# Performance work log

Hardware: AMD Instinct MI355X
Metric: run time of the kernel (lower is better)

## Reference

```python
import jax, jax.numpy as jnp
import numpy as np

N, E, F_IN, G = 50000, 800000, 128, 256
LAYERS = [(128, 4, 64), (256, 4, 64), (256, 1, 64)]  # (fan_in, heads, per-head dim)


def setup_inputs() -> dict:
    key = jax.random.key(0)
    ks = iter(jax.random.split(key, 64))
    nrm = lambda shp, s=1.0: jax.random.normal(next(ks), shp, jnp.float32) * s
    d = {}
    d["x"] = nrm((N, F_IN))
    d["edge_index"] = jax.random.randint(next(ks), (2, E), 0, N, dtype=jnp.int32)
    d["batch"] = jnp.sort(jax.random.randint(next(ks), (N,), 0, G, dtype=jnp.int32))
    for i, (fin, h, c) in enumerate(LAYERS):
        d[f"w{i}"] = nrm((fin, h * c), 1.0 / np.sqrt(fin))
        d[f"asrc{i}"] = nrm((h, c), 0.1)
        d[f"adst{i}"] = nrm((h, c), 0.1)
        d[f"b{i}"] = nrm((h * c,), 0.1)
        d[f"g{i}"] = 1.0 + nrm((h * c,), 0.1)
        d[f"be{i}"] = nrm((h * c,), 0.1)
        d[f"m{i}"] = nrm((h * c,), 0.1)
        d[f"v{i}"] = jnp.abs(nrm((h * c,), 0.1)) + 1.0
    d["fc1w"] = nrm((192, 64), 1.0 / np.sqrt(192)); d["fc1b"] = nrm((64,), 0.1)
    d["fc2w"] = nrm((64, 32), 1.0 / np.sqrt(64));   d["fc2b"] = nrm((32,), 0.1)
    d["fc3w"] = nrm((32, 1), 1.0 / np.sqrt(32));    d["fc3b"] = nrm((1,), 0.1)
    return d


def _gat_layer(x, w, a_s, a_d, b, src, dst, n, heads):
    c = w.shape[1] // heads
    h = (x @ w).reshape(n, heads, c)                      # [N,H,C]
    al_s = jnp.sum(h * a_s[None], axis=-1)                # [N,H]
    al_d = jnp.sum(h * a_d[None], axis=-1)                # [N,H]
    e = jax.nn.leaky_relu(al_s[src] + al_d[dst], 0.2)     # [E',H]
    emax = jax.ops.segment_max(e, dst, num_segments=n)
    emax = jnp.where(jnp.isfinite(emax), emax, 0.0)
    ee = jnp.exp(e - emax[dst])
    den = jax.ops.segment_sum(ee, dst, num_segments=n)
    alpha = ee / (den[dst] + 1e-16)                       # edge softmax per dst node
    out = jax.ops.segment_sum(h[src] * alpha[..., None], dst, num_segments=n)
    return out.reshape(n, heads * c) + b


def _bn(x, g, be, m, v):
    return (x - m) * jax.lax.rsqrt(v + 1e-5) * g + be


def reference(x, edge_index, batch,
              w0, asrc0, adst0, b0, g0, be0, m0, v0,
              w1, asrc1, adst1, b1, g1, be1, m1, v1,
              w2, asrc2, adst2, b2, g2, be2, m2, v2,
              fc1w, fc1b, fc2w, fc2b, fc3w, fc3b):
    n = x.shape[0]
    loop = jnp.arange(n, dtype=edge_index.dtype)          # add_self_loops (PyG default)
    src = jnp.concatenate([edge_index[0], loop])
    dst = jnp.concatenate([edge_index[1], loop])
    layers = [(w0, asrc0, adst0, b0, g0, be0, m0, v0, 4),
              (w1, asrc1, adst1, b1, g1, be1, m1, v1, 4),
              (w2, asrc2, adst2, b2, g2, be2, m2, v2, 1)]
    for (w, a_s, a_d, b, g, be, m, v, heads) in layers:
        x = _gat_layer(x, w, a_s, a_d, b, src, dst, n, heads)
        x = jax.nn.elu(_bn(x, g, be, m, v))
    # multi-pool readout over graphs
    xsum = jax.ops.segment_sum(x, batch, num_segments=G)
    cnt = jax.ops.segment_sum(jnp.ones((n, 1), x.dtype), batch, num_segments=G)
    xmean = xsum / jnp.maximum(cnt, 1.0)
    xmax = jax.ops.segment_max(x, batch, num_segments=G)
    xmax = jnp.where(jnp.isfinite(xmax), xmax, 0.0)
    h = jnp.concatenate([xmean, xmax, xsum], axis=1)      # [G, 192]
    h = jax.nn.relu(h @ fc1w + fc1b)
    h = jax.nn.relu(h @ fc2w + fc2b)
    return h @ fc3w + fc3b                                # [G, 1]
```

## Files before the change

kernel.cpp:

```cpp
#include <hip/hip_runtime.h>
#include <hip/hip_fp16.h>

typedef unsigned short ushort_t;
typedef unsigned int uint_t;
typedef __attribute__((ext_vector_type(8))) _Float16 half8;
typedef __attribute__((ext_vector_type(4))) float f32x4;

#define NN 50000
#define NE 800000
#define NGR 256

typedef __attribute__((address_space(3))) unsigned int as3_u32;
typedef const __attribute__((address_space(1))) unsigned int as1_u32c;
__device__ __forceinline__ void gld16(const ushort_t* g, void* lds_base) {
    __builtin_amdgcn_global_load_lds((as1_u32c*)g, (as3_u32*)lds_base, 16, 0, 0);
}

__global__ void k_scan1(const int* __restrict__ deg, int* __restrict__ rowp,
                        int* __restrict__ bsum, int M) {
    __shared__ int sm[256];
    int t = threadIdx.x, i = blockIdx.x * 256 + t;
    int v = (i < M) ? deg[i] + 1 : 0;
    sm[t] = v; __syncthreads();
    for (int off = 1; off < 256; off <<= 1) {
        int x = (t >= off) ? sm[t - off] : 0;
        __syncthreads();
        sm[t] += x;
        __syncthreads();
    }
    if (i < M) rowp[i] = sm[t] - v;
    if (t == 255) bsum[blockIdx.x] = sm[255];
}

__global__ void k_scan2(int* bsum, int NB) {
    __shared__ int sm[256];
    int t = threadIdx.x;
    int v = (t < NB) ? bsum[t] : 0;
    sm[t] = v; __syncthreads();
    for (int off = 1; off < 256; off <<= 1) {
        int x = (t >= off) ? sm[t - off] : 0;
        __syncthreads();
        sm[t] += x;
        __syncthreads();
    }
    if (t < NB) bsum[t] = sm[t] - v;
}

__global__ void k_scan3(int* rowp, const int* __restrict__ bsum, int* __restrict__ cur,
                        int M, int total) {
    int i = blockIdx.x * 256 + threadIdx.x;
    if (i < M) { rowp[i] += bsum[blockIdx.x]; cur[i] = 0; }
    if (i == 0) rowp[M] = total;
}

__global__ void k_prep(const float* __restrict__ x0, __half* __restrict__ xf,
                       const float* __restrict__ W0, const float* __restrict__ W1,
                       const float* __restrict__ W2, __half* __restrict__ th,
                       const int* __restrict__ edst, int* __restrict__ deg) {
    int i = blockIdx.x * 256 + threadIdx.x;
    if (i < 1600000) {
        float4 v = ((const float4*)x0)[i];
        __half2 a = __floats2half2_rn(v.x, v.y);
        __half2 b = __floats2half2_rn(v.z, v.w);
        *(__half2*)(xf + i * 4) = a;
        *(__half2*)(xf + i * 4 + 2) = b;
    } else if (i < 1600000 + 114688) {
        int w = i - 1600000;
        const float* W; int K, NC, idx, base;
        if (w < 32768)      { W = W0; K = 128; NC = 256; idx = w;         base = 0; }
        else if (w < 98304) { W = W1; K = 256; NC = 256; idx = w - 32768; base = 32768; }
        else                { W = W2; K = 256; NC = 64;  idx = w - 98304; base = 98304; }
        int k = idx / NC, n = idx % NC;
        th[base + n * K + k] = __float2half(W[idx]);
    } else if (i < 1600000 + 114688 + NE) {
        atomicAdd(&deg[edst[i - 1714688]], 1);
    }
}

template<int KD, int BN>
__device__ __forceinline__ void gemm_body(int bx, int by,
    const __half* __restrict__ Ax, const __half* __restrict__ Bth,
    __half* __restrict__ Hout, const float* __restrict__ a_s,
    const float* __restrict__ a_d, float* __restrict__ als,
    float* __restrict__ ald, int H, int M, int NC) {
    constexpr int BM = 128, BK = 32;
    __shared__ ushort_t sA[BM * BK];
    __shared__ ushort_t sB[BN * BK];
    const int tid = threadIdx.x;
    const int m0 = bx * BM;
    const int n0 = by * BN;
    const int wv = tid >> 6, ln = tid & 63;
    const int lrow = ln & 15, lq = ln >> 4;
    constexpr int RT = (BN == 128) ? 4 : 2;
    int wm, wn;
    if constexpr (BN == 128) { wm = (wv >> 1) * 64; wn = (wv & 1) * 64; }
    else                     { wm = wv * 32;        wn = 0; }
    const int roff = ln >> 2;
    const int coff = (ln & 3) * 8;

    f32x4 acc[RT][4] = {};

    for (int k0 = 0; k0 < KD; k0 += BK) {
        #pragma unroll
        for (int ch = 0; ch < 2; ++ch) {
            int rb = wv * 32 + ch * 16;
            size_t ga = (size_t)(m0 + rb + roff) * KD + k0 + coff;
            gld16((const ushort_t*)Ax + ga, &sA[rb * BK]);
        }
        if constexpr (BN == 128) {
            #pragma unroll
            for (int ch = 0; ch < 2; ++ch) {
                int rb = wv * 32 + ch * 16;
                size_t gb = (size_t)(n0 + rb + roff) * KD + k0 + coff;
                gld16((const ushort_t*)Bth + gb, &sB[rb * BK]);
            }
        } else {
            int rb = wv * 16;
            size_t gb = (size_t)(n0 + rb + roff) * KD + k0 + coff;
            gld16((const ushort_t*)Bth + gb, &sB[rb * BK]);
        }
        __syncthreads();
        half8 af[RT], bf[4];
        #pragma unroll
        for (int r = 0; r < RT; ++r)
            af[r] = *(const half8*)&sA[(wm + r * 16 + lrow) * BK + lq * 8];
        #pragma unroll
        for (int c = 0; c < 4; ++c)
            bf[c] = *(const half8*)&sB[(wn + c * 16 + lrow) * BK + lq * 8];
        #pragma unroll
        for (int r = 0; r < RT; ++r)
            #pragma unroll
            for (int c = 0; c < 4; ++c)
                acc[r][c] = __builtin_amdgcn_mfma_f32_16x16x32_f16(af[r], bf[c], acc[r][c], 0, 0, 0);
        __syncthreads();
    }
    #pragma unroll
    for (int r = 0; r < RT; ++r) {
        #pragma unroll
        for (int c = 0; c < 4; ++c) {
            int colg = n0 + wn + c * 16 + lrow;
            #pragma unroll
            for (int j = 0; j < 4; ++j) {
                int row = m0 + wm + r * 16 + lq * 4 + j;
                if (row < M) Hout[(size_t)row * NC + colg] = __float2half(acc[r][c][j]);
            }
        }
    }
    int hh = (n0 + wn) >> 6;
    float asv[4], adv[4];
    #pragma unroll
    for (int c = 0; c < 4; ++c) {
        int cg = (n0 + wn + c * 16 + lrow) & 63;
        asv[c] = a_s[hh * 64 + cg];
        adv[c] = a_d[hh * 64 + cg];
    }
    #pragma unroll
    for (int r = 0; r < RT; ++r) {
        #pragma unroll
        for (int j = 0; j < 4; ++j) {
            float ts = 0.f, td = 0.f;
            #pragma unroll
            for (int c = 0; c < 4; ++c) {
                float v = acc[r][c][j];
                ts += v * asv[c];
                td += v * adv[c];
            }
            #pragma unroll
            for (int m = 1; m < 16; m <<= 1) {
                ts += __shfl_xor(ts, m);
                td += __shfl_xor(td, m);
            }
            int row = m0 + wm + r * 16 + lq * 4 + j;
            if (lrow == 0 && row < M) {
                als[row * H + hh] = ts;
                ald[row * H + hh] = td;
            }
        }
    }
}

template<int KD, int BN>
__global__ __launch_bounds__(256)
void k_mgemm(const __half* __restrict__ Ax, const __half* __restrict__ Bth,
             __half* __restrict__ Hout,
             const float* __restrict__ a_s, const float* __restrict__ a_d,
             float* __restrict__ als, float* __restrict__ ald,
             int H, int M, int NC) {
    gemm_body<KD, BN>(blockIdx.x, blockIdx.y, Ax, Bth, Hout, a_s, a_d, als, ald, H, M, NC);
}

__global__ __launch_bounds__(256)
void k_gf(const __half* __restrict__ Ax, const __half* __restrict__ Bth,
          __half* __restrict__ Hout,
          const float* __restrict__ a_s, const float* __restrict__ a_d,
          float* __restrict__ als, float* __restrict__ ald, int M,
          const int* __restrict__ esrc, const int* __restrict__ edst,
          const int* __restrict__ rowp, int* __restrict__ cur,
          int* __restrict__ colv) {
    if (blockIdx.x < 782) {
        gemm_body<128, 128>(blockIdx.x >> 1, blockIdx.x & 1, Ax, Bth, Hout,
                            a_s, a_d, als, ald, 4, M, 256);
    } else {
        int i = (blockIdx.x - 782) * 256 + threadIdx.x;
        if (i < NE) {
            int d = edst[i];
            int pos = rowp[d] + atomicAdd(&cur[d], 1);
            colv[pos] = esrc[i];
        } else if (i < NE + NN) {
            int nn = i - NE;
            int pos = rowp[nn] + atomicAdd(&cur[nn], 1);
            colv[pos] = nn;
        }
    }
}

template<int H>
__global__ __launch_bounds__(256)
void k_att(const float* __restrict__ als, const float* __restrict__ ald,
           const int* __restrict__ rowp, const int* __restrict__ colv,
           __half* __restrict__ alpha, float* __restrict__ invb, int M) {
    int node = blockIdx.x * 16 + (threadIdx.x >> 4);
    if (node >= M) return;
    int l = threadIdx.x & 15;
    int rs = rowp[node], re = rowp[node + 1];
    if constexpr (H == 4) {
        float4 ad = *(const float4*)(ald + node * 4);
        float d0 = 0.f, d1 = 0.f, d2 = 0.f, d3 = 0.f;
        for (int i = rs + l; i < re; i += 16) {
            int s = colv[i];
            float4 av = *(const float4*)(als + s * 4);
            float e0 = av.x + ad.x; e0 = e0 > 0.f ? e0 : 0.2f * e0; e0 = __expf(e0);
            float e1 = av.y + ad.y; e1 = e1 > 0.f ? e1 : 0.2f * e1; e1 = __expf(e1);
            float e2 = av.z + ad.z; e2 = e2 > 0.f ? e2 : 0.2f * e2; e2 = __expf(e2);
            float e3 = av.w + ad.w; e3 = e3 > 0.f ? e3 : 0.2f * e3; e3 = __expf(e3);
            d0 += e0; d1 += e1; d2 += e2; d3 += e3;
            __half2 p0 = __floats2half2_rn(e0, e1);
            __half2 p1 = __floats2half2_rn(e2, e3);
            uint2 pk;
            pk.x = *(uint_t*)&p0; pk.y = *(uint_t*)&p1;
            *(uint2*)(alpha + (size_t)i * 4) = pk;
        }
        #pragma unroll
        for (int off = 1; off < 16; off <<= 1) {
            d0 += __shfl_xor(d0, off); d1 += __shfl_xor(d1, off);
            d2 += __shfl_xor(d2, off); d3 += __shfl_xor(d3, off);
        }
        if (l == 0)
            *(float4*)(invb + node * 4) = make_float4(1.f / (d0 + 1e-16f), 1.f / (d1 + 1e-16f),
                                                      1.f / (d2 + 1e-16f), 1.f / (d3 + 1e-16f));
    } else {
        float ad = ald[node];
        float d = 0.f;
        for (int i = rs + l; i < re; i += 16) {
            int s = colv[i];
            float e = als[s] + ad; e = e > 0.f ? e : 0.2f * e; e = __expf(e);
            d += e;
            alpha[i] = __float2half(e);
        }
        #pragma unroll
        for (int off = 1; off < 16; off <<= 1) d += __shfl_xor(d, off);
        if (l == 0) invb[node] = 1.f / (d + 1e-16f);
    }
}

template<int H, bool SPLIT>
__global__ __launch_bounds__(256)
void k_agg(const __half* __restrict__ h, const __half* __restrict__ alpha,
           const float* __restrict__ invb, const int* __restrict__ rowp,
           const int* __restrict__ colv,
           const float* __restrict__ bias, const float* __restrict__ gam,
           const float* __restrict__ bet, const float* __restrict__ mu,
           const float* __restrict__ var,
           __half* __restrict__ xo, float* __restrict__ xf, int M) {
    constexpr int HC = H * 64;
    constexpr int EG = 512 / HC;
    constexpr int L  = 64 / EG;
    constexpr int UN = (H == 4) ? 4 : 2;
    int node = blockIdx.x * 4 + (threadIdx.x >> 6);
    if (node >= M) return;
    int lane = threadIdx.x & 63;
    int rs = rowp[node], re = rowp[node + 1];
    int l = lane & (L - 1), eg = lane / L;
    int hB = (l * 8) >> 6;
    const ushort_t* ab = (const ushort_t*)alpha;
    float acc[8] = {};
    for (int i = rs; i < re; i += EG * UN) {
        #pragma unroll
        for (int k = 0; k < UN; ++k) {
            int idx = i + eg + k * EG;
            bool vld = idx < re;
            int idx2 = vld ? idx : rs;
            int s = colv[idx2];
            ushort_t abits;
            if constexpr (H == 4) abits = ab[(size_t)idx2 * 4 + hB];
            else                  abits = ab[idx2];
            float a = __half2float(__ushort_as_half(vld ? abits : (ushort_t)0));
            uint4 hv = *(const uint4*)(h + (size_t)s * HC + l * 8);
            const __half* hp = (const __half*)&hv;
            #pragma unroll
            for (int j = 0; j < 8; ++j)
                acc[j] = fmaf(a, __half2float(hp[j]), acc[j]);
        }
    }
    #pragma unroll
    for (int off = L; off < 64; off <<= 1) {
        #pragma unroll
        for (int j = 0; j < 8; ++j) acc[j] += __shfl_xor(acc[j], off);
    }
    if (eg == 0) {
        float inv = (H == 4) ? invb[node * 4 + hB] : invb[node];
        float fo[8];
        #pragma unroll
        for (int j = 0; j < 8; ++j) {
            int d = l * 8 + j;
            float o = acc[j] * inv + bias[d];
            float bn = (o - mu[d]) * rsqrtf(var[d] + 1e-5f) * gam[d] + bet[d];
            fo[j] = bn > 0.f ? bn : (__expf(bn) - 1.f);
        }
        if constexpr (SPLIT) {
            __half2 p0 = __floats2half2_rn(fo[0], fo[1]);
            __half2 p1 = __floats2half2_rn(fo[2], fo[3]);
            __half2 p2 = __floats2half2_rn(fo[4], fo[5]);
            __half2 p3 = __floats2half2_rn(fo[6], fo[7]);
            uint4 pk;
            pk.x = *(uint_t*)&p0; pk.y = *(uint_t*)&p1;
            pk.z = *(uint_t*)&p2; pk.w = *(uint_t*)&p3;
            *(uint4*)&xo[(size_t)node * HC + l * 8] = pk;
        } else {
            *(float4*)&xf[(size_t)node * HC + l * 8] = make_float4(fo[0], fo[1], fo[2], fo[3]);
            *(float4*)&xf[(size_t)node * HC + l * 8 + 4] = make_float4(fo[4], fo[5], fo[6], fo[7]);
        }
    }
}

__global__ __launch_bounds__(512)
void k_poolfc(const float* __restrict__ x, const int* __restrict__ batch,
              const float* __restrict__ fc1w, const float* __restrict__ fc1b,
              const float* __restrict__ fc2w, const float* __restrict__ fc2b,
              const float* __restrict__ fc3w, const float* __restrict__ fc3b,
              float* __restrict__ out, int M) {
    __shared__ float ssum[8][64];
    __shared__ float smax[8][64];
    __shared__ float hb[192];
    __shared__ float h1[64];
    __shared__ float h2[32];
    int g = blockIdx.x, t = threadIdx.x;
    int d = t & 63, sub = t >> 6;
    int lo = 0, hi = M;
    while (lo < hi) { int mid = (lo + hi) >> 1; if (batch[mid] < g) lo = mid + 1; else hi = mid; }
    int s = lo;
    lo = 0; hi = M;
    while (lo < hi) { int mid = (lo + hi) >> 1; if (batch[mid] < g + 1) lo = mid + 1; else hi = mid; }
    int e = lo;
    float sum = 0.f, mx = -3.0e38f;
    for (int n = s + sub; n < e; n += 8) {
        float v = x[(size_t)n * 64 + d];
        sum += v; mx = fmaxf(mx, v);
    }
    ssum[sub][d] = sum; smax[sub][d] = mx;
    __syncthreads();
    if (t < 64) {
        float sm = 0.f, m2 = -3.0e38f;
        #pragma unroll
        for (int k = 0; k < 8; ++k) { sm += ssum[k][t]; m2 = fmaxf(m2, smax[k][t]); }
        int cnt = e - s;
        hb[t] = sm / (float)(cnt > 1 ? cnt : 1);
        hb[64 + t] = (cnt == 0) ? 0.f : m2;
        hb[128 + t] = sm;
    }
    __syncthreads();
    if (t < 64) {
        float s1 = fc1b[t];
        for (int k = 0; k < 192; ++k) s1 += hb[k] * fc1w[k * 64 + t];
        h1[t] = fmaxf(s1, 0.f);
    }
    __syncthreads();
    if (t < 32) {
        float s2 = fc2b[t];
        for (int k = 0; k < 64; ++k) s2 += h1[k] * fc2w[k * 32 + t];
        h2[t] = fmaxf(s2, 0.f);
    }
    __syncthreads();
    if (t == 0) {
        float s3 = fc3b[0];
        for (int k = 0; k < 32; ++k) s3 += h2[k] * fc3w[k];
        out[g] = s3;
    }
}

extern "C" void kernel_launch(void* const* d_in, const int* in_sizes, int n_in,
                              void* d_out, int out_size, void* d_ws, size_t ws_size,
                              hipStream_t stream) {
    const float* x0     = (const float*)d_in[0];
    const int* ei       = (const int*)d_in[1];
    const int* batch    = (const int*)d_in[2];
    const float* W[3]   = {(const float*)d_in[3],  (const float*)d_in[11], (const float*)d_in[19]};
    const float* AS[3]  = {(const float*)d_in[4],  (const float*)d_in[12], (const float*)d_in[20]};
    const float* AD[3]  = {(const float*)d_in[5],  (const float*)d_in[13], (const float*)d_in[21]};
    const float* BI[3]  = {(const float*)d_in[6],  (const float*)d_in[14], (const float*)d_in[22]};
    const float* GA[3]  = {(const float*)d_in[7],  (const float*)d_in[15], (const float*)d_in[23]};
    const float* BE[3]  = {(const float*)d_in[8],  (const float*)d_in[16], (const float*)d_in[24]};
    const float* MU[3]  = {(const float*)d_in[9],  (const float*)d_in[17], (const float*)d_in[25]};
    const float* VA[3]  = {(const float*)d_in[10], (const float*)d_in[18], (const float*)d_in[26]};
    const float* fc1w = (const float*)d_in[27];
    const float* fc1b = (const float*)d_in[28];
    const float* fc2w = (const float*)d_in[29];
    const float* fc2b = (const float*)d_in[30];
    const float* fc3w = (const float*)d_in[31];
    const float* fc3b = (const float*)d_in[32];

    char* ws = (char*)d_ws;
    int*   rowp   = (int*)  (ws);
    int*   colv   = (int*)  (ws + 200704);
    int*   bsum   = (int*)  (ws + 3600704);
    float* als    = (float*)(ws + 3602432);
    float* ald    = (float*)(ws + 4402432);
    __half* wTh   = (__half*)(ws + 5202432);
    __half* h_buf = (__half*)(ws + 5661184);
    __half* xf16  = (__half*)(ws + 31261184);
    float* xpool  = (float*)(ws + 56885760);
    __half* alpha = (__half*)(ws + 69685760);
    float* invb   = (float*)(ws + 83285760);
    int*   cur    = (int*)  (ws + 84085760);

    const int* esrc = ei;
    const int* edst = ei + NE;
    const int NB_SCAN = (NN + 255) / 256;

    hipMemsetAsync(cur, 0, NN * sizeof(int), stream);
    k_prep<<<(1600000 + 114688 + NE + 255) / 256, 256, 0, stream>>>(x0, xf16, W[0], W[1], W[2],
                                                                    wTh, edst, cur);
    k_scan1<<<NB_SCAN, 256, 0, stream>>>(cur, rowp, bsum, NN);
    k_scan2<<<1, 256, 0, stream>>>(bsum, NB_SCAN);
    k_scan3<<<NB_SCAN, 256, 0, stream>>>(rowp, bsum, cur, NN, NE + NN);

    const int GB = (NN + 127) / 128;
    const int FILLB = (NE + NN + 255) / 256;
    int nwb = (NN + 3) / 4;
    int nab = (NN + 15) / 16;

    k_gf<<<782 + FILLB, 256, 0, stream>>>(xf16, wTh, h_buf, AS[0], AD[0], als, ald, NN,
                                          esrc, edst, rowp, cur, colv);
    k_att<4><<<nab, 256, 0, stream>>>(als, ald, rowp, colv, alpha, invb, NN);
    k_agg<4, true><<<nwb, 256, 0, stream>>>(h_buf, alpha, invb, rowp, colv,
                                            BI[0], GA[0], BE[0], MU[0], VA[0],
                                            xf16, nullptr, NN);
    k_mgemm<256, 128><<<dim3(GB, 2), 256, 0, stream>>>(xf16, wTh + 32768, h_buf,
                                                       AS[1], AD[1], als, ald, 4, NN, 256);
    k_att<4><<<nab, 256, 0, stream>>>(als, ald, rowp, colv, alpha, invb, NN);
    k_agg<4, true><<<nwb, 256, 0, stream>>>(h_buf, alpha, invb, rowp, colv,
                                            BI[1], GA[1], BE[1], MU[1], VA[1],
                                            xf16, nullptr, NN);
    k_mgemm<256, 64><<<dim3(GB, 1), 256, 0, stream>>>(xf16, wTh + 98304, h_buf,
                                                      AS[2], AD[2], als, ald, 1, NN, 64);
    k_att<1><<<nab, 256, 0, stream>>>(als, ald, rowp, colv, alpha, invb, NN);
    k_agg<1, false><<<nwb, 256, 0, stream>>>(h_buf, alpha, invb, rowp, colv,
                                             BI[2], GA[2], BE[2], MU[2], VA[2],
                                             nullptr, xpool, NN);

    k_poolfc<<<NGR, 512, 0, stream>>>(xpool, batch, fc1w, fc1b, fc2w, fc2b, fc3w, fc3b,
                                      (float*)d_out, NN);
    (void)in_sizes; (void)n_in; (void)out_size; (void)ws_size;
}
```

Measured before the change: 453.4 us.

## Fuse edge-softmax attention into aggregation kernel using per-wave LDS alpha cache

```diff
diff --git a/kernel.cpp b/kernel.cpp
--- a/kernel.cpp
+++ b/kernel.cpp
@@ -214,59 +214,11 @@
     }
 }
 
-template<int H>
-__global__ __launch_bounds__(256)
-void k_att(const float* __restrict__ als, const float* __restrict__ ald,
-           const int* __restrict__ rowp, const int* __restrict__ colv,
-           __half* __restrict__ alpha, float* __restrict__ invb, int M) {
-    int node = blockIdx.x * 16 + (threadIdx.x >> 4);
-    if (node >= M) return;
-    int l = threadIdx.x & 15;
-    int rs = rowp[node], re = rowp[node + 1];
-    if constexpr (H == 4) {
-        float4 ad = *(const float4*)(ald + node * 4);
-        float d0 = 0.f, d1 = 0.f, d2 = 0.f, d3 = 0.f;
-        for (int i = rs + l; i < re; i += 16) {
-            int s = colv[i];
-            float4 av = *(const float4*)(als + s * 4);
-            float e0 = av.x + ad.x; e0 = e0 > 0.f ? e0 : 0.2f * e0; e0 = __expf(e0);
-            float e1 = av.y + ad.y; e1 = e1 > 0.f ? e1 : 0.2f * e1; e1 = __expf(e1);
-            float e2 = av.z + ad.z; e2 = e2 > 0.f ? e2 : 0.2f * e2; e2 = __expf(e2);
-            float e3 = av.w + ad.w; e3 = e3 > 0.f ? e3 : 0.2f * e3; e3 = __expf(e3);
-            d0 += e0; d1 += e1; d2 += e2; d3 += e3;
-            __half2 p0 = __floats2half2_rn(e0, e1);
-            __half2 p1 = __floats2half2_rn(e2, e3);
-            uint2 pk;
-            pk.x = *(uint_t*)&p0; pk.y = *(uint_t*)&p1;
-            *(uint2*)(alpha + (size_t)i * 4) = pk;
-        }
-        #pragma unroll
-        for (int off = 1; off < 16; off <<= 1) {
-            d0 += __shfl_xor(d0, off); d1 += __shfl_xor(d1, off);
-            d2 += __shfl_xor(d2, off); d3 += __shfl_xor(d3, off);
-        }
-        if (l == 0)
-            *(float4*)(invb + node * 4) = make_float4(1.f / (d0 + 1e-16f), 1.f / (d1 + 1e-16f),
-                                                      1.f / (d2 + 1e-16f), 1.f / (d3 + 1e-16f));
-    } else {
-        float ad = ald[node];
-        float d = 0.f;
-        for (int i = rs + l; i < re; i += 16) {
-            int s = colv[i];
-            float e = als[s] + ad; e = e > 0.f ? e : 0.2f * e; e = __expf(e);
-            d += e;
-            alpha[i] = __float2half(e);
-        }
-        #pragma unroll
-        for (int off = 1; off < 16; off <<= 1) d += __shfl_xor(d, off);
-        if (l == 0) invb[node] = 1.f / (d + 1e-16f);
-    }
-}
-
+#define CAP 192
 template<int H, bool SPLIT>
 __global__ __launch_bounds__(256)
-void k_agg(const __half* __restrict__ h, const __half* __restrict__ alpha,
-           const float* __restrict__ invb, const int* __restrict__ rowp,
+void k_agg(const __half* __restrict__ h, const float* __restrict__ als,
+           const float* __restrict__ ald, const int* __restrict__ rowp,
            const int* __restrict__ colv,
            const float* __restrict__ bias, const float* __restrict__ gam,
            const float* __restrict__ bet, const float* __restrict__ mu,
@@ -276,13 +228,58 @@
     constexpr int EG = 512 / HC;
     constexpr int L  = 64 / EG;
     constexpr int UN = (H == 4) ? 4 : 2;
+    __shared__ ushort_t alf[4][CAP * H];
     int node = blockIdx.x * 4 + (threadIdx.x >> 6);
     if (node >= M) return;
+    int w = threadIdx.x >> 6;
     int lane = threadIdx.x & 63;
     int rs = rowp[node], re = rowp[node + 1];
     int l = lane & (L - 1), eg = lane / L;
     int hB = (l * 8) >> 6;
-    const ushort_t* ab = (const ushort_t*)alpha;
+    float inv, adB;
+    if constexpr (H == 4) {
+        float4 ad4 = *(const float4*)(ald + node * 4);
+        float d0 = 0.f, d1 = 0.f, d2 = 0.f, d3 = 0.f;
+        for (int i = rs + lane; i < re; i += 64) {
+            int s = colv[i];
+            float4 av = *(const float4*)(als + s * 4);
+            float e0 = av.x + ad4.x; e0 = e0 > 0.f ? e0 : 0.2f * e0; e0 = __expf(e0);
+            float e1 = av.y + ad4.y; e1 = e1 > 0.f ? e1 : 0.2f * e1; e1 = __expf(e1);
+            float e2 = av.z + ad4.z; e2 = e2 > 0.f ? e2 : 0.2f * e2; e2 = __expf(e2);
+            float e3 = av.w + ad4.w; e3 = e3 > 0.f ? e3 : 0.2f * e3; e3 = __expf(e3);
+            d0 += e0; d1 += e1; d2 += e2; d3 += e3;
+            int o = i - rs;
+            if (o < CAP) {
+                __half2 p0 = __floats2half2_rn(e0, e1);
+                __half2 p1 = __floats2half2_rn(e2, e3);
+                uint2 pk;
+                pk.x = *(uint_t*)&p0; pk.y = *(uint_t*)&p1;
+                *(uint2*)&alf[w][o * 4] = pk;
+            }
+        }
+        #pragma unroll
+        for (int off = 1; off < 64; off <<= 1) {
+            d0 += __shfl_xor(d0, off); d1 += __shfl_xor(d1, off);
+            d2 += __shfl_xor(d2, off); d3 += __shfl_xor(d3, off);
+        }
+        float den = (hB == 0) ? d0 : (hB == 1) ? d1 : (hB == 2) ? d2 : d3;
+        inv = 1.f / (den + 1e-16f);
+        adB = ((const float*)&ad4)[hB];
+    } else {
+        float ad = ald[node];
+        float d = 0.f;
+        for (int i = rs + lane; i < re; i += 64) {
+            int s = colv[i];
+            float e = als[s] + ad; e = e > 0.f ? e : 0.2f * e; e = __expf(e);
+            d += e;
+            int o = i - rs;
+            if (o < CAP) alf[w][o] = __half_as_ushort(__float2half(e));
+        }
+        #pragma unroll
+        for (int off = 1; off < 64; off <<= 1) d += __shfl_xor(d, off);
+        inv = 1.f / (d + 1e-16f);
+        adB = ad;
+    }
     float acc[8] = {};
     for (int i = rs; i < re; i += EG * UN) {
         #pragma unroll
@@ -291,10 +288,19 @@
             bool vld = idx < re;
             int idx2 = vld ? idx : rs;
             int s = colv[idx2];
-            ushort_t abits;
-            if constexpr (H == 4) abits = ab[(size_t)idx2 * 4 + hB];
-            else                  abits = ab[idx2];
-            float a = __half2float(__ushort_as_half(vld ? abits : (ushort_t)0));
+            int o = idx2 - rs;
+            float a;
+            if (o < CAP) {
+                ushort_t abits;
+                if constexpr (H == 4) abits = alf[w][o * 4 + hB];
+                else                  abits = alf[w][o];
+                a = __half2float(__ushort_as_half(abits));
+            } else {
+                float e = ((H == 4) ? als[s * 4 + hB] : als[s]) + adB;
+                e = e > 0.f ? e : 0.2f * e;
+                a = __expf(e);
+            }
+            a = vld ? a : 0.f;
             uint4 hv = *(const uint4*)(h + (size_t)s * HC + l * 8);
             const __half* hp = (const __half*)&hv;
             #pragma unroll
@@ -308,7 +314,6 @@
         for (int j = 0; j < 8; ++j) acc[j] += __shfl_xor(acc[j], off);
     }
     if (eg == 0) {
-        float inv = (H == 4) ? invb[node * 4 + hB] : invb[node];
         float fo[8];
         #pragma unroll
         for (int j = 0; j < 8; ++j) {
@@ -419,9 +424,7 @@
     __half* h_buf = (__half*)(ws + 5661184);
     __half* xf16  = (__half*)(ws + 31261184);
     float* xpool  = (float*)(ws + 56885760);
-    __half* alpha = (__half*)(ws + 69685760);
-    float* invb   = (float*)(ws + 83285760);
-    int*   cur    = (int*)  (ws + 84085760);
+    int*   cur    = (int*)  (ws + 69685760);
 
     const int* esrc = ei;
     const int* edst = ei + NE;
@@ -437,24 +440,20 @@
     const int GB = (NN + 127) / 128;
     const int FILLB = (NE + NN + 255) / 256;
     int nwb = (NN + 3) / 4;
-    int nab = (NN + 15) / 16;
 
     k_gf<<<782 + FILLB, 256, 0, stream>>>(xf16, wTh, h_buf, AS[0], AD[0], als, ald, NN,
                                           esrc, edst, rowp, cur, colv);
-    k_att<4><<<nab, 256, 0, stream>>>(als, ald, rowp, colv, alpha, invb, NN);
-    k_agg<4, true><<<nwb, 256, 0, stream>>>(h_buf, alpha, invb, rowp, colv,
+    k_agg<4, true><<<nwb, 256, 0, stream>>>(h_buf, als, ald, rowp, colv,
                                             BI[0], GA[0], BE[0], MU[0], VA[0],
                                             xf16, nullptr, NN);
     k_mgemm<256, 128><<<dim3(GB, 2), 256, 0, stream>>>(xf16, wTh + 32768, h_buf,
                                                        AS[1], AD[1], als, ald, 4, NN, 256);
-    k_att<4><<<nab, 256, 0, stream>>>(als, ald, rowp, colv, alpha, invb, NN);
-    k_agg<4, true><<<nwb, 256, 0, stream>>>(h_buf, alpha, invb, rowp, colv,
+    k_agg<4, true><<<nwb, 256, 0, stream>>>(h_buf, als, ald, rowp, colv,
                                             BI[1], GA[1], BE[1], MU[1], VA[1],
                                             xf16, nullptr, NN);
     k_mgemm<256, 64><<<dim3(GB, 1), 256, 0, stream>>>(xf16, wTh + 98304, h_buf,
                                                       AS[2], AD[2], als, ald, 1, NN, 64);
-    k_att<1><<<nab, 256, 0, stream>>>(als, ald, rowp, colv, alpha, invb, NN);
-    k_agg<1, false><<<nwb, 256, 0, stream>>>(h_buf, alpha, invb, rowp, colv,
+    k_agg<1, false><<<nwb, 256, 0, stream>>>(h_buf, als, ald, rowp, colv,
                                              BI[2], GA[2], BE[2], MU[2], VA[2],
                                              nullptr, xpool, NN);
 
```

After: 499.2 us. 10.1% more time.
